# Kernel tuning notes

Hardware: AMD Instinct MI355X
Metric: run time of the kernel (lower is better)

## Reference

```python
import jax, jax.numpy as jnp
import numpy as np

N_NODES = 100000
N_EDGES = 3200000
NEG_SLOPE = 0.2  # PyG GATConv default


def setup_inputs() -> dict:
    key = jax.random.key(0)
    ks = jax.random.split(key, 10)
    x = jax.random.normal(ks[0], (N_NODES, 2), dtype=jnp.float32)
    src = jax.random.randint(ks[1], (N_EDGES,), 0, N_NODES)
    dst = jax.random.randint(ks[2], (N_EDGES,), 0, N_NODES)
    edge_index = jnp.stack([src, dst]).astype(jnp.int64)
    edge_attr = jax.random.normal(ks[3], (N_EDGES, 4), dtype=jnp.float32)
    # layer 1: in=2, heads=4, out_per_head=8
    W1 = jax.random.normal(ks[4], (2, 32), dtype=jnp.float32) * 0.5
    att_src1 = jax.random.normal(ks[5], (4, 8), dtype=jnp.float32) * 0.3
    att_dst1 = jax.random.normal(ks[6], (4, 8), dtype=jnp.float32) * 0.3
    b1 = jnp.zeros((32,), dtype=jnp.float32)
    # layer 2: in=32, heads=1, out_per_head=2
    W2 = jax.random.normal(ks[7], (32, 2), dtype=jnp.float32) * 0.2
    att_src2 = jax.random.normal(ks[8], (1, 2), dtype=jnp.float32) * 0.3
    att_dst2 = jax.random.normal(ks[9], (1, 2), dtype=jnp.float32) * 0.3
    b2 = jnp.zeros((2,), dtype=jnp.float32)
    return {"x": x, "edge_index": edge_index, "edge_attr": edge_attr,
            "W1": W1, "att_src1": att_src1, "att_dst1": att_dst1, "b1": b1,
            "W2": W2, "att_src2": att_src2, "att_dst2": att_dst2, "b2": b2}


def _gat_conv(x, W, att_src, att_dst, bias, src, dst, heads, out_ch, concat, n):
    h = (x @ W).reshape(n, heads, out_ch)            # [N,H,C]
    a_s = (h * att_src).sum(-1)                       # [N,H]
    a_d = (h * att_dst).sum(-1)                       # [N,H]
    e = jax.nn.leaky_relu(a_s[src] + a_d[dst], NEG_SLOPE)  # [E,H]
    m = jax.ops.segment_max(e, dst, num_segments=n)   # stable softmax over dst groups
    ee = jnp.exp(e - m[dst])
    s = jax.ops.segment_sum(ee, dst, num_segments=n)
    alpha = ee / (s[dst] + 1e-16)                     # [E,H]
    out = jax.ops.segment_sum(h[src] * alpha[:, :, None], dst, num_segments=n)  # [N,H,C]
    out = out.reshape(n, heads * out_ch) if concat else out.mean(axis=1)
    return out + bias, alpha


def reference(x, edge_index, edge_attr, W1, att_src1, att_dst1, b1,
              W2, att_src2, att_dst2, b2):
    # edge_attr is accepted but ignored: GATConv was built without edge_dim.
    n = x.shape[0]
    loop = jnp.arange(n, dtype=edge_index.dtype)      # add_self_loops=True (PyG default)
    src = jnp.concatenate([edge_index[0], loop])
    dst = jnp.concatenate([edge_index[1], loop])
    h, alpha1 = _gat_conv(x, W1, att_src1, att_dst1, b1, src, dst, 4, 8, True, n)
    h = jax.nn.elu(h)
    out, alpha2 = _gat_conv(h, W2, att_src2, att_dst2, b2, src, dst, 1, 2, False, n)
    return out, alpha1, alpha2
```

## Files before the change

kernel.cpp:

```cpp
#include <hip/hip_runtime.h>
#include <hip/hip_fp16.h>
#include <math.h>

#define NEG_SLOPE 0.2f
#define BW 512
#define BSH 9
#define CAP 18432
#define NB_MAX 256

typedef float f4v __attribute__((ext_vector_type(4)));
typedef float f2v __attribute__((ext_vector_type(2)));
typedef int   i2v __attribute__((ext_vector_type(2)));

__device__ __forceinline__ float lrelu(float v) {
    return v > 0.0f ? v : NEG_SLOPE * v;
}
__device__ __forceinline__ float pack2h(float a, float b) {
    __half2 h = __floats2half2_rn(a, b);
    return *reinterpret_cast<float*>(&h);
}
__device__ __forceinline__ float2 unpack2h(float f) {
    __half2 h = *reinterpret_cast<__half2*>(&f);
    return __half22float2(h);
}
__device__ __forceinline__ void nt_store4(float4 v, float4* p) {
    f4v x = {v.x, v.y, v.z, v.w};
    __builtin_nontemporal_store(x, (f4v*)p);
}
__device__ __forceinline__ void nt_store2(float2 v, float2* p) {
    f2v x = {v.x, v.y};
    __builtin_nontemporal_store(x, (f2v*)p);
}

__global__ __launch_bounds__(256) void k_l1_node(
    const float* __restrict__ x, const float* __restrict__ W1,
    const float* __restrict__ asw, const float* __restrict__ adw,
    float4* __restrict__ ga, float4* __restrict__ spack,
    float2* __restrict__ dpack2, int* __restrict__ bucketCursor,
    int nb, int n)
{
    int i = blockIdx.x * blockDim.x + threadIdx.x;
    if (i < nb) bucketCursor[i] = 0;
    if (i >= n) return;
    float2 xv = ((const float2*)x)[i];
    float as[4] = {0.f, 0.f, 0.f, 0.f};
    float ad[4] = {0.f, 0.f, 0.f, 0.f};
    #pragma unroll
    for (int j = 0; j < 32; ++j) {
        float h = xv.x * W1[j] + xv.y * W1[32 + j];
        as[j >> 3] += h * asw[j];
        ad[j >> 3] += h * adw[j];
    }
    float p01 = pack2h(as[0], as[1]), p23 = pack2h(as[2], as[3]);
    ga[i] = make_float4(p01, p23, xv.x, xv.y);
    spack[i] = make_float4(p01, p23, 0.f, 0.f);
    dpack2[2 * i] = make_float2(pack2h(ad[0], ad[1]), pack2h(ad[2], ad[3]));
}

__global__ __launch_bounds__(256) void k_binA(
    const int* __restrict__ ei, int* __restrict__ bucketCursor,
    unsigned int* __restrict__ binned, int E, int Et, int nb)
{
    __shared__ int cnt[NB_MAX], lscan[NB_MAX], base[NB_MAX], lcur[NB_MAX];
    __shared__ unsigned int staging[4096];
    __shared__ short sbk[4096];
    int t = threadIdx.x;
    int c0 = blockIdx.x * 4096;
    unsigned int ent[16];
    short bb[16];
    #pragma unroll
    for (int k = 0; k < 16; ++k) {
        int e = c0 + k * 256 + t;
        int s, d;
        if (e < E) {
            s = __builtin_nontemporal_load(&ei[e]);
            d = __builtin_nontemporal_load(&ei[E + e]);
        } else { s = e - E; d = s; }
        bool valid = e < Et;
        bb[k] = valid ? (short)(d >> BSH) : (short)(-1);
        ent[k] = ((unsigned int)s << BSH) | (unsigned int)(d & (BW - 1));
    }
    cnt[t] = 0;
    __syncthreads();
    #pragma unroll
    for (int k = 0; k < 16; ++k)
        if (bb[k] >= 0) atomicAdd(&cnt[bb[k]], 1);
    __syncthreads();
    int c = cnt[t];
    lscan[t] = c;
    __syncthreads();
    for (int off = 1; off < 256; off <<= 1) {
        int v = (t >= off) ? lscan[t - off] : 0;
        __syncthreads();
        lscan[t] += v;
        __syncthreads();
    }
    int tot = lscan[255];
    int ex = lscan[t] - c;
    __syncthreads();
    lscan[t] = ex;
    lcur[t] = ex;
    if (t < nb && c > 0) base[t] = atomicAdd(&bucketCursor[t], c);
    __syncthreads();
    #pragma unroll
    for (int k = 0; k < 16; ++k)
        if (bb[k] >= 0) {
            int p = atomicAdd(&lcur[bb[k]], 1);
            staging[p] = ent[k];
            sbk[p] = bb[k];
        }
    __syncthreads();
    for (int j = t; j < tot; j += 256) {
        int lo = sbk[j];
        __builtin_nontemporal_store(staging[j],
            &binned[(size_t)lo * CAP + base[lo] + (j - lscan[lo])]);
    }
}

__global__ __launch_bounds__(1024) void k_binB(
    const unsigned int* __restrict__ binned, const int* __restrict__ bucketCursor,
    int* __restrict__ sorted, int2* __restrict__ rowrange, int n, int nb)
{
    __shared__ int cnt[BW], cur[BW];
    int t = threadIdx.x;
    int b = blockIdx.x;
    int m = bucketCursor[b];
    size_t base = (size_t)b * CAP;
    int node0 = b << BSH;
    if (t < BW) cnt[t] = 0;
    __syncthreads();
    for (int i = t; i < m; i += 1024)
        atomicAdd(&cnt[binned[base + i] & (BW - 1)], 1);
    __syncthreads();
    int deg = (t < BW) ? cnt[t] : 0;
    for (int off = 1; off < BW; off <<= 1) {
        int v = (t >= off && t < BW) ? cnt[t - off] : 0;
        __syncthreads();
        if (t < BW) cnt[t] += v;
        __syncthreads();
    }
    if (t < BW) {
        int ex = cnt[t] - deg;
        cur[t] = ex;
        int node = node0 + t;
        if (node < n)
            rowrange[node] = make_int2((int)base + ex, (int)base + ex + deg);
    }
    __syncthreads();
    for (int i = t; i < m; i += 1024) {
        unsigned int en = binned[base + i];
        int dl = (int)(en & (BW - 1));
        int p = atomicAdd(&cur[dl], 1);
        sorted[base + p] = (int)(en >> BSH);
    }
}

__global__ __launch_bounds__(256) void k_l1_gather(
    const int2* __restrict__ rowrange, const int* __restrict__ sorted,
    const float4* __restrict__ ga, float2* __restrict__ dpack2,
    const float* __restrict__ W1, const float* __restrict__ b1,
    const float* __restrict__ W2,
    const float* __restrict__ asw2, const float* __restrict__ adw2,
    float4* __restrict__ pk2f, float4* __restrict__ spack,
    __half* __restrict__ dpk2h, int n)
{
    int t = blockIdx.x * blockDim.x + threadIdx.x;
    int d = t >> 1, half = t & 1;
    if (d >= n) return;
    int2 rr = rowrange[d];
    int beg = rr.x, end = rr.y;
    float2 adp = dpack2[2 * d];
    float2 ad01 = unpack2h(adp.x), ad23 = unpack2h(adp.y);
    float see[4] = {0.f, 0.f, 0.f, 0.f};
    float sx0[4] = {0.f, 0.f, 0.f, 0.f};
    float sx1[4] = {0.f, 0.f, 0.f, 0.f};
    int i = beg + half;
    for (; i + 2 < end; i += 4) {
        int s0 = sorted[i], s1 = sorted[i + 2];
        float4 v0 = ga[s0], v1 = ga[s1];
        #pragma unroll
        for (int k = 0; k < 2; ++k) {
            float4 v = k ? v1 : v0;
            float2 a01 = unpack2h(v.x), a23 = unpack2h(v.y);
            float e0 = __expf(lrelu(a01.x + ad01.x));
            float e1 = __expf(lrelu(a01.y + ad01.y));
            float e2 = __expf(lrelu(a23.x + ad23.x));
            float e3 = __expf(lrelu(a23.y + ad23.y));
            see[0] += e0; sx0[0] += e0 * v.z; sx1[0] += e0 * v.w;
            see[1] += e1; sx0[1] += e1 * v.z; sx1[1] += e1 * v.w;
            see[2] += e2; sx0[2] += e2 * v.z; sx1[2] += e2 * v.w;
            see[3] += e3; sx0[3] += e3 * v.z; sx1[3] += e3 * v.w;
        }
    }
    for (; i < end; i += 2) {
        float4 v = ga[sorted[i]];
        float2 a01 = unpack2h(v.x), a23 = unpack2h(v.y);
        float e0 = __expf(lrelu(a01.x + ad01.x));
        float e1 = __expf(lrelu(a01.y + ad01.y));
        float e2 = __expf(lrelu(a23.x + ad23.x));
        float e3 = __expf(lrelu(a23.y + ad23.y));
        see[0] += e0; sx0[0] += e0 * v.z; sx1[0] += e0 * v.w;
        see[1] += e1; sx0[1] += e1 * v.z; sx1[1] += e1 * v.w;
        see[2] += e2; sx0[2] += e2 * v.z; sx1[2] += e2 * v.w;
        see[3] += e3; sx0[3] += e3 * v.z; sx1[3] += e3 * v.w;
    }
    #pragma unroll
    for (int h = 0; h < 4; ++h) {
        see[h] += __shfl_xor(see[h], 1);
        sx0[h] += __shfl_xor(sx0[h], 1);
        sx1[h] += __shfl_xor(sx1[h], 1);
    }
    if (half) return;
    float rs[4];
    #pragma unroll
    for (int h = 0; h < 4; ++h) rs[h] = 1.0f / (see[h] + 1e-16f);
    dpack2[2 * d + 1] = make_float2(pack2h(rs[0], rs[1]), pack2h(rs[2], rs[3]));
    float h20 = 0.f, h21 = 0.f;
    #pragma unroll
    for (int j = 0; j < 32; ++j) {
        int h = j >> 3;
        float num = W1[j] * sx0[h] + W1[32 + j] * sx1[h];
        float o = num * rs[h] + b1[j];
        float he = o > 0.f ? o : expm1f(o);
        h20 += he * W2[2 * j];
        h21 += he * W2[2 * j + 1];
    }
    float as2 = h20 * asw2[0] + h21 * asw2[1];
    float ad2 = h20 * adw2[0] + h21 * adw2[1];
    pk2f[d] = make_float4(as2, h20, h21, ad2);
    ((float*)&spack[d])[2] = as2;
    dpk2h[2 * d] = __float2half(ad2);
}

__global__ __launch_bounds__(256) void k_l2_gather(
    const int2* __restrict__ rowrange, const int* __restrict__ sorted,
    const float4* __restrict__ pk2f, const float* __restrict__ b2,
    __half* __restrict__ dpk2h, float* __restrict__ out, int n)
{
    int t = blockIdx.x * blockDim.x + threadIdx.x;
    int d = t >> 1, half = t & 1;
    if (d >= n) return;
    int2 rr = rowrange[d];
    int beg = rr.x, end = rr.y;
    float ad2 = pk2f[d].w;
    float se = 0.f, a0 = 0.f, a1 = 0.f;
    int i = beg + half;
    for (; i + 2 < end; i += 4) {
        int s0 = sorted[i], s1 = sorted[i + 2];
        float4 p0 = pk2f[s0], p1 = pk2f[s1];
        float e0 = __expf(lrelu(p0.x + ad2));
        float e1 = __expf(lrelu(p1.x + ad2));
        se += e0 + e1;
        a0 += e0 * p0.y + e1 * p1.y;
        a1 += e0 * p0.z + e1 * p1.z;
    }
    for (; i < end; i += 2) {
        float4 p = pk2f[sorted[i]];
        float ee = __expf(lrelu(p.x + ad2));
        se += ee; a0 += ee * p.y; a1 += ee * p.z;
    }
    se += __shfl_xor(se, 1);
    a0 += __shfl_xor(a0, 1);
    a1 += __shfl_xor(a1, 1);
    if (half) return;
    float rs2 = 1.0f / (se + 1e-16f);
    dpk2h[2 * d + 1] = __float2half(rs2);
    ((float2*)out)[d] = make_float2(a0 * rs2 + b2[0], a1 * rs2 + b2[1]);
}

__global__ __launch_bounds__(256) void k_alpha(
    const int* __restrict__ ei, const float4* __restrict__ spack,
    const float4* __restrict__ dpack, const float* __restrict__ dpk2hf,
    float4* __restrict__ alpha1, float2* __restrict__ alpha2_2, int E, int Et)
{
    int p = blockIdx.x * blockDim.x + threadIdx.x;
    int e0 = p * 2;
    if (e0 >= Et) return;
    int s0, d0, s1, d1;
    if (e0 < E) {
        i2v ss = __builtin_nontemporal_load(&((const i2v*)ei)[p]);
        i2v dd = __builtin_nontemporal_load((const i2v*)(ei + E) + (p - E / 2) + E / 2 - E / 2 + (p - 0) - p + p);
        dd = __builtin_nontemporal_load((const i2v*)(ei + E) + p);
        s0 = ss.x; s1 = ss.y; d0 = dd.x; d1 = dd.y;
    } else {
        s0 = e0 - E; d0 = s0; s1 = s0 + 1; d1 = s1;
    }
    float4 sp0 = spack[s0], sp1 = spack[s1];
    float4 dp0 = dpack[d0], dp1 = dpack[d1];
    float  dh0 = dpk2hf[d0], dh1 = dpk2hf[d1];

    float2 a01, a23, b01, b23, r01, r23, ar;
    float4 al;
    a01 = unpack2h(sp0.x); a23 = unpack2h(sp0.y);
    b01 = unpack2h(dp0.x); b23 = unpack2h(dp0.y);
    r01 = unpack2h(dp0.z); r23 = unpack2h(dp0.w);
    al.x = __expf(lrelu(a01.x + b01.x)) * r01.x;
    al.y = __expf(lrelu(a01.y + b01.y)) * r01.y;
    al.z = __expf(lrelu(a23.x + b23.x)) * r23.x;
    al.w = __expf(lrelu(a23.y + b23.y)) * r23.y;
    nt_store4(al, &alpha1[e0]);
    ar = unpack2h(dh0);
    float o20 = __expf(lrelu(sp0.z + ar.x)) * ar.y;
    a01 = unpack2h(sp1.x); a23 = unpack2h(sp1.y);
    b01 = unpack2h(dp1.x); b23 = unpack2h(dp1.y);
    r01 = unpack2h(dp1.z); r23 = unpack2h(dp1.w);
    al.x = __expf(lrelu(a01.x + b01.x)) * r01.x;
    al.y = __expf(lrelu(a01.y + b01.y)) * r01.y;
    al.z = __expf(lrelu(a23.x + b23.x)) * r23.x;
    al.w = __expf(lrelu(a23.y + b23.y)) * r23.y;
    nt_store4(al, &alpha1[e0 + 1]);
    ar = unpack2h(dh1);
    float o21 = __expf(lrelu(sp1.z + ar.x)) * ar.y;
    nt_store2(make_float2(o20, o21), &alpha2_2[p]);
}

extern "C" void kernel_launch(void* const* d_in, const int* in_sizes, int n_in,
                              void* d_out, int out_size, void* d_ws, size_t ws_size,
                              hipStream_t stream)
{
    const float* x   = (const float*)d_in[0];
    const int*   ei  = (const int*)d_in[1];
    const float* W1  = (const float*)d_in[3];
    const float* as1 = (const float*)d_in[4];
    const float* ad1 = (const float*)d_in[5];
    const float* b1  = (const float*)d_in[6];
    const float* W2  = (const float*)d_in[7];
    const float* as2 = (const float*)d_in[8];
    const float* ad2 = (const float*)d_in[9];
    const float* b2  = (const float*)d_in[10];

    const int n  = in_sizes[0] / 2;
    const int E  = in_sizes[1] / 2;
    const int Et = E + n;
    const int nb = (n + BW - 1) >> BSH;

    char* w = (char*)d_ws;
    float4* ga    = (float4*)w;  w += (size_t)n * sizeof(float4);
    float4* spack = (float4*)w;  w += (size_t)n * sizeof(float4);
    float4* dpack = (float4*)w;  w += (size_t)n * sizeof(float4);
    float4* pk2f  = (float4*)w;  w += (size_t)n * sizeof(float4);
    float*  dpk2hf= (float*)w;   w += (size_t)n * sizeof(float);
    int2*   rowrange = (int2*)w; w += (size_t)n * sizeof(int2);
    int*    sorted   = (int*)w;  w += (size_t)nb * CAP * sizeof(int);
    int*    bucketCursor = (int*)w; w += (size_t)nb * sizeof(int);

    float*  out    = (float*)d_out;
    float4* alpha1 = (float4*)(out + (size_t)n * 2);
    float2* alpha2_2 = (float2*)(alpha1 + (size_t)Et);
    unsigned int* binned = (unsigned int*)alpha1;

    dim3 blk(256);
    int gn   = (n + 255) / 256;
    int gn2  = (2 * n + 255) / 256;
    int gA   = (Et + 4095) / 4096;
    int gP   = (Et / 2 + 255) / 256;

    k_l1_node  <<<gn,  blk, 0, stream>>>(x, W1, as1, ad1, ga, spack,
                                         (float2*)dpack, bucketCursor, nb, n);
    k_binA     <<<gA,  blk, 0, stream>>>(ei, bucketCursor, binned, E, Et, nb);
    k_binB     <<<nb, dim3(1024), 0, stream>>>(binned, bucketCursor, sorted, rowrange, n, nb);
    k_l1_gather<<<gn2, blk, 0, stream>>>(rowrange, sorted, ga, (float2*)dpack,
                                         W1, b1, W2, as2, ad2, pk2f, spack,
                                         (__half*)dpk2hf, n);
    k_l2_gather<<<gn2, blk, 0, stream>>>(rowrange, sorted, pk2f, b2,
                                         (__half*)dpk2hf, out, n);
    k_alpha    <<<gP,  blk, 0, stream>>>(ei, spack, dpack, dpk2hf,
                                         alpha1, alpha2_2, E, Et);
}
```

Before: 291.6 us.

## Merge per-destination alpha data into one 32-byte record and stage alpha1 stores through LDS

Combines the destination-side layer-1 record (attention logits plus reciprocal sums) and the layer-2 dst logit/reciprocal into one 32-byte per-node record. The layer-2 pair is now stored in fp32 rather than half. Each random gather in k_alpha then touches one contiguous region instead of two separate arrays. k_alpha also writes its alpha1 results to shared memory and then stores them so consecutive lanes write consecutive float4s. The cost is a doubled dpk footprint, a block barrier and some LDS traffic.

```diff
diff --git a/kernel.cpp b/kernel.cpp
--- a/kernel.cpp
+++ b/kernel.cpp
@@ -36,7 +36,7 @@
     const float* __restrict__ x, const float* __restrict__ W1,
     const float* __restrict__ asw, const float* __restrict__ adw,
     float4* __restrict__ ga, float4* __restrict__ spack,
-    float2* __restrict__ dpack2, int* __restrict__ bucketCursor,
+    float4* __restrict__ dpk, int* __restrict__ bucketCursor,
     int nb, int n)
 {
     int i = blockIdx.x * blockDim.x + threadIdx.x;
@@ -54,7 +54,7 @@
     float p01 = pack2h(as[0], as[1]), p23 = pack2h(as[2], as[3]);
     ga[i] = make_float4(p01, p23, xv.x, xv.y);
     spack[i] = make_float4(p01, p23, 0.f, 0.f);
-    dpack2[2 * i] = make_float2(pack2h(ad[0], ad[1]), pack2h(ad[2], ad[3]));
+    dpk[2 * i] = make_float4(pack2h(ad[0], ad[1]), pack2h(ad[2], ad[3]), 0.f, 0.f);
 }
 
 __global__ __launch_bounds__(256) void k_binA(
@@ -157,19 +157,18 @@
 
 __global__ __launch_bounds__(256) void k_l1_gather(
     const int2* __restrict__ rowrange, const int* __restrict__ sorted,
-    const float4* __restrict__ ga, float2* __restrict__ dpack2,
+    const float4* __restrict__ ga, float4* __restrict__ dpk,
     const float* __restrict__ W1, const float* __restrict__ b1,
     const float* __restrict__ W2,
     const float* __restrict__ asw2, const float* __restrict__ adw2,
-    float4* __restrict__ pk2f, float4* __restrict__ spack,
-    __half* __restrict__ dpk2h, int n)
+    float4* __restrict__ pk2f, float4* __restrict__ spack, int n)
 {
     int t = blockIdx.x * blockDim.x + threadIdx.x;
     int d = t >> 1, half = t & 1;
     if (d >= n) return;
     int2 rr = rowrange[d];
     int beg = rr.x, end = rr.y;
-    float2 adp = dpack2[2 * d];
+    float2 adp = *(const float2*)&dpk[2 * d];
     float2 ad01 = unpack2h(adp.x), ad23 = unpack2h(adp.y);
     float see[4] = {0.f, 0.f, 0.f, 0.f};
     float sx0[4] = {0.f, 0.f, 0.f, 0.f};
@@ -214,7 +213,7 @@
     float rs[4];
     #pragma unroll
     for (int h = 0; h < 4; ++h) rs[h] = 1.0f / (see[h] + 1e-16f);
-    dpack2[2 * d + 1] = make_float2(pack2h(rs[0], rs[1]), pack2h(rs[2], rs[3]));
+    ((float2*)&dpk[2 * d])[1] = make_float2(pack2h(rs[0], rs[1]), pack2h(rs[2], rs[3]));
     float h20 = 0.f, h21 = 0.f;
     #pragma unroll
     for (int j = 0; j < 32; ++j) {
@@ -229,13 +228,13 @@
     float ad2 = h20 * adw2[0] + h21 * adw2[1];
     pk2f[d] = make_float4(as2, h20, h21, ad2);
     ((float*)&spack[d])[2] = as2;
-    dpk2h[2 * d] = __float2half(ad2);
+    ((float*)&dpk[2 * d + 1])[0] = ad2;
 }
 
 __global__ __launch_bounds__(256) void k_l2_gather(
     const int2* __restrict__ rowrange, const int* __restrict__ sorted,
     const float4* __restrict__ pk2f, const float* __restrict__ b2,
-    __half* __restrict__ dpk2h, float* __restrict__ out, int n)
+    float4* __restrict__ dpk, float* __restrict__ out, int n)
 {
     int t = blockIdx.x * blockDim.x + threadIdx.x;
     int d = t >> 1, half = t & 1;
@@ -264,54 +263,62 @@
     a1 += __shfl_xor(a1, 1);
     if (half) return;
     float rs2 = 1.0f / (se + 1e-16f);
-    dpk2h[2 * d + 1] = __float2half(rs2);
+    ((float*)&dpk[2 * d + 1])[1] = rs2;
     ((float2*)out)[d] = make_float2(a0 * rs2 + b2[0], a1 * rs2 + b2[1]);
 }
 
 __global__ __launch_bounds__(256) void k_alpha(
     const int* __restrict__ ei, const float4* __restrict__ spack,
-    const float4* __restrict__ dpack, const float* __restrict__ dpk2hf,
+    const float4* __restrict__ dpk,
     float4* __restrict__ alpha1, float2* __restrict__ alpha2_2, int E, int Et)
 {
-    int p = blockIdx.x * blockDim.x + threadIdx.x;
-    int e0 = p * 2;
-    if (e0 >= Et) return;
-    int s0, d0, s1, d1;
-    if (e0 < E) {
-        i2v ss = __builtin_nontemporal_load(&((const i2v*)ei)[p]);
-        i2v dd = __builtin_nontemporal_load((const i2v*)(ei + E) + (p - E / 2) + E / 2 - E / 2 + (p - 0) - p + p);
-        dd = __builtin_nontemporal_load((const i2v*)(ei + E) + p);
-        s0 = ss.x; s1 = ss.y; d0 = dd.x; d1 = dd.y;
-    } else {
-        s0 = e0 - E; d0 = s0; s1 = s0 + 1; d1 = s1;
-    }
-    float4 sp0 = spack[s0], sp1 = spack[s1];
-    float4 dp0 = dpack[d0], dp1 = dpack[d1];
-    float  dh0 = dpk2hf[d0], dh1 = dpk2hf[d1];
-
-    float2 a01, a23, b01, b23, r01, r23, ar;
-    float4 al;
-    a01 = unpack2h(sp0.x); a23 = unpack2h(sp0.y);
-    b01 = unpack2h(dp0.x); b23 = unpack2h(dp0.y);
-    r01 = unpack2h(dp0.z); r23 = unpack2h(dp0.w);
-    al.x = __expf(lrelu(a01.x + b01.x)) * r01.x;
-    al.y = __expf(lrelu(a01.y + b01.y)) * r01.y;
-    al.z = __expf(lrelu(a23.x + b23.x)) * r23.x;
-    al.w = __expf(lrelu(a23.y + b23.y)) * r23.y;
-    nt_store4(al, &alpha1[e0]);
-    ar = unpack2h(dh0);
-    float o20 = __expf(lrelu(sp0.z + ar.x)) * ar.y;
-    a01 = unpack2h(sp1.x); a23 = unpack2h(sp1.y);
-    b01 = unpack2h(dp1.x); b23 = unpack2h(dp1.y);
-    r01 = unpack2h(dp1.z); r23 = unpack2h(dp1.w);
-    al.x = __expf(lrelu(a01.x + b01.x)) * r01.x;
-    al.y = __expf(lrelu(a01.y + b01.y)) * r01.y;
-    al.z = __expf(lrelu(a23.x + b23.x)) * r23.x;
-    al.w = __expf(lrelu(a23.y + b23.y)) * r23.y;
-    nt_store4(al, &alpha1[e0 + 1]);
-    ar = unpack2h(dh1);
-    float o21 = __expf(lrelu(sp1.z + ar.x)) * ar.y;
-    nt_store2(make_float2(o20, o21), &alpha2_2[p]);
+    __shared__ float4 lds[512];
+    int t = threadIdx.x;
+    int base = blockIdx.x * 512;
+    int e0 = base + 2 * t;
+    if (e0 < Et) {
+        int s0, d0, s1, d1;
+        if (e0 < E) {
+            i2v ss = __builtin_nontemporal_load((const i2v*)(ei + e0));
+            i2v dd = __builtin_nontemporal_load((const i2v*)(ei + E + e0));
+            s0 = ss.x; s1 = ss.y; d0 = dd.x; d1 = dd.y;
+        } else {
+            s0 = e0 - E; d0 = s0; s1 = s0 + 1; d1 = s1;
+        }
+        float4 sp0 = spack[s0], sp1 = spack[s1];
+        float4 dA0 = dpk[2 * d0], dA1 = dpk[2 * d1];
+        float2 dB0 = *(const float2*)&dpk[2 * d0 + 1];
+        float2 dB1 = *(const float2*)&dpk[2 * d1 + 1];
+
+        float2 a01, a23, b01, b23, r01, r23;
+        float4 al;
+        a01 = unpack2h(sp0.x); a23 = unpack2h(sp0.y);
+        b01 = unpack2h(dA0.x); b23 = unpack2h(dA0.y);
+        r01 = unpack2h(dA0.z); r23 = unpack2h(dA0.w);
+        al.x = __expf(lrelu(a01.x + b01.x)) * r01.x;
+        al.y = __expf(lrelu(a01.y + b01.y)) * r01.y;
+        al.z = __expf(lrelu(a23.x + b23.x)) * r23.x;
+        al.w = __expf(lrelu(a23.y + b23.y)) * r23.y;
+        lds[t] = al;
+        float o20 = __expf(lrelu(sp0.z + dB0.x)) * dB0.y;
+        a01 = unpack2h(sp1.x); a23 = unpack2h(sp1.y);
+        b01 = unpack2h(dA1.x); b23 = unpack2h(dA1.y);
+        r01 = unpack2h(dA1.z); r23 = unpack2h(dA1.w);
+        al.x = __expf(lrelu(a01.x + b01.x)) * r01.x;
+        al.y = __expf(lrelu(a01.y + b01.y)) * r01.y;
+        al.z = __expf(lrelu(a23.x + b23.x)) * r23.x;
+        al.w = __expf(lrelu(a23.y + b23.y)) * r23.y;
+        lds[256 + t] = al;
+        float o21 = __expf(lrelu(sp1.z + dB1.x)) * dB1.y;
+        nt_store2(make_float2(o20, o21), &alpha2_2[(base >> 1) + t]);
+    }
+    __syncthreads();
+    int v0 = t;
+    if (base + v0 < Et)
+        nt_store4(lds[(v0 & 1) * 256 + (v0 >> 1)], &alpha1[base + v0]);
+    int v1 = t + 256;
+    if (base + v1 < Et)
+        nt_store4(lds[(v1 & 1) * 256 + 128 + (v1 >> 1) - 128], &alpha1[base + v1]);
 }
 
 extern "C" void kernel_launch(void* const* d_in, const int* in_sizes, int n_in,
@@ -337,9 +344,8 @@
     char* w = (char*)d_ws;
     float4* ga    = (float4*)w;  w += (size_t)n * sizeof(float4);
     float4* spack = (float4*)w;  w += (size_t)n * sizeof(float4);
-    float4* dpack = (float4*)w;  w += (size_t)n * sizeof(float4);
+    float4* dpk   = (float4*)w;  w += (size_t)n * 2 * sizeof(float4);
     float4* pk2f  = (float4*)w;  w += (size_t)n * sizeof(float4);
-    float*  dpk2hf= (float*)w;   w += (size_t)n * sizeof(float);
     int2*   rowrange = (int2*)w; w += (size_t)n * sizeof(int2);
     int*    sorted   = (int*)w;  w += (size_t)nb * CAP * sizeof(int);
     int*    bucketCursor = (int*)w; w += (size_t)nb * sizeof(int);
@@ -353,17 +359,16 @@
     int gn   = (n + 255) / 256;
     int gn2  = (2 * n + 255) / 256;
     int gA   = (Et + 4095) / 4096;
-    int gP   = (Et / 2 + 255) / 256;
+    int gAl  = (Et + 511) / 512;
 
     k_l1_node  <<<gn,  blk, 0, stream>>>(x, W1, as1, ad1, ga, spack,
-                                         (float2*)dpack, bucketCursor, nb, n);
+                                         dpk, bucketCursor, nb, n);
     k_binA     <<<gA,  blk, 0, stream>>>(ei, bucketCursor, binned, E, Et, nb);
     k_binB     <<<nb, dim3(1024), 0, stream>>>(binned, bucketCursor, sorted, rowrange, n, nb);
-    k_l1_gather<<<gn2, blk, 0, stream>>>(rowrange, sorted, ga, (float2*)dpack,
-                                         W1, b1, W2, as2, ad2, pk2f, spack,
-                                         (__half*)dpk2hf, n);
+    k_l1_gather<<<gn2, blk, 0, stream>>>(rowrange, sorted, ga, dpk,
+                                         W1, b1, W2, as2, ad2, pk2f, spack, n);
     k_l2_gather<<<gn2, blk, 0, stream>>>(rowrange, sorted, pk2f, b2,
-                                         (__half*)dpk2hf, out, n);
-    k_alpha    <<<gP,  blk, 0, stream>>>(ei, spack, dpack, dpk2hf,
+                                         dpk, out, n);
+    k_alpha    <<<gAl, blk, 0, stream>>>(ei, spack, dpk,
                                          alpha1, alpha2_2, E, Et);
 }
```

After: 289.7 us. No clear change (-0.7%).

## Use 8 lanes per node in gathers and stage alpha1 stores through LDS

Applied to the files above, without the earlier changes.

Both gather kernels now give each destination node 8 lanes instead of 2 and reduce the partial sums with three xor-shuffle steps. This spreads the ~33 edges per node across more threads for more memory-level parallelism. The alpha kernel now writes alpha1 into shared memory first and then issues contiguous, coalesced float4 nontemporal stores, instead of each thread storing to two strided positions. The costs are 4x more threads in the gathers, extra shuffle work, and a block barrier plus 8KB of LDS in the alpha kernel.

```diff
diff --git a/kernel.cpp b/kernel.cpp
--- a/kernel.cpp
+++ b/kernel.cpp
@@ -165,7 +165,7 @@
     __half* __restrict__ dpk2h, int n)
 {
     int t = blockIdx.x * blockDim.x + threadIdx.x;
-    int d = t >> 1, half = t & 1;
+    int d = t >> 3, q = t & 7;
     if (d >= n) return;
     int2 rr = rowrange[d];
     int beg = rr.x, end = rr.y;
@@ -174,9 +174,9 @@
     float see[4] = {0.f, 0.f, 0.f, 0.f};
     float sx0[4] = {0.f, 0.f, 0.f, 0.f};
     float sx1[4] = {0.f, 0.f, 0.f, 0.f};
-    int i = beg + half;
-    for (; i + 2 < end; i += 4) {
-        int s0 = sorted[i], s1 = sorted[i + 2];
+    int i = beg + q;
+    for (; i + 8 < end; i += 16) {
+        int s0 = sorted[i], s1 = sorted[i + 8];
         float4 v0 = ga[s0], v1 = ga[s1];
         #pragma unroll
         for (int k = 0; k < 2; ++k) {
@@ -192,7 +192,7 @@
             see[3] += e3; sx0[3] += e3 * v.z; sx1[3] += e3 * v.w;
         }
     }
-    for (; i < end; i += 2) {
+    for (; i < end; i += 8) {
         float4 v = ga[sorted[i]];
         float2 a01 = unpack2h(v.x), a23 = unpack2h(v.y);
         float e0 = __expf(lrelu(a01.x + ad01.x));
@@ -209,8 +209,14 @@
         see[h] += __shfl_xor(see[h], 1);
         sx0[h] += __shfl_xor(sx0[h], 1);
         sx1[h] += __shfl_xor(sx1[h], 1);
-    }
-    if (half) return;
+        see[h] += __shfl_xor(see[h], 2);
+        sx0[h] += __shfl_xor(sx0[h], 2);
+        sx1[h] += __shfl_xor(sx1[h], 2);
+        see[h] += __shfl_xor(see[h], 4);
+        sx0[h] += __shfl_xor(sx0[h], 4);
+        sx1[h] += __shfl_xor(sx1[h], 4);
+    }
+    if (q) return;
     float rs[4];
     #pragma unroll
     for (int h = 0; h < 4; ++h) rs[h] = 1.0f / (see[h] + 1e-16f);
@@ -238,15 +244,15 @@
     __half* __restrict__ dpk2h, float* __restrict__ out, int n)
 {
     int t = blockIdx.x * blockDim.x + threadIdx.x;
-    int d = t >> 1, half = t & 1;
+    int d = t >> 3, q = t & 7;
     if (d >= n) return;
     int2 rr = rowrange[d];
     int beg = rr.x, end = rr.y;
     float ad2 = pk2f[d].w;
     float se = 0.f, a0 = 0.f, a1 = 0.f;
-    int i = beg + half;
-    for (; i + 2 < end; i += 4) {
-        int s0 = sorted[i], s1 = sorted[i + 2];
+    int i = beg + q;
+    for (; i + 8 < end; i += 16) {
+        int s0 = sorted[i], s1 = sorted[i + 8];
         float4 p0 = pk2f[s0], p1 = pk2f[s1];
         float e0 = __expf(lrelu(p0.x + ad2));
         float e1 = __expf(lrelu(p1.x + ad2));
@@ -254,15 +260,15 @@
         a0 += e0 * p0.y + e1 * p1.y;
         a1 += e0 * p0.z + e1 * p1.z;
     }
-    for (; i < end; i += 2) {
+    for (; i < end; i += 8) {
         float4 p = pk2f[sorted[i]];
         float ee = __expf(lrelu(p.x + ad2));
         se += ee; a0 += ee * p.y; a1 += ee * p.z;
     }
-    se += __shfl_xor(se, 1);
-    a0 += __shfl_xor(a0, 1);
-    a1 += __shfl_xor(a1, 1);
-    if (half) return;
+    se += __shfl_xor(se, 1); a0 += __shfl_xor(a0, 1); a1 += __shfl_xor(a1, 1);
+    se += __shfl_xor(se, 2); a0 += __shfl_xor(a0, 2); a1 += __shfl_xor(a1, 2);
+    se += __shfl_xor(se, 4); a0 += __shfl_xor(a0, 4); a1 += __shfl_xor(a1, 4);
+    if (q) return;
     float rs2 = 1.0f / (se + 1e-16f);
     dpk2h[2 * d + 1] = __float2half(rs2);
     ((float2*)out)[d] = make_float2(a0 * rs2 + b2[0], a1 * rs2 + b2[1]);
@@ -273,45 +279,54 @@
     const float4* __restrict__ dpack, const float* __restrict__ dpk2hf,
     float4* __restrict__ alpha1, float2* __restrict__ alpha2_2, int E, int Et)
 {
-    int p = blockIdx.x * blockDim.x + threadIdx.x;
-    int e0 = p * 2;
-    if (e0 >= Et) return;
-    int s0, d0, s1, d1;
-    if (e0 < E) {
-        i2v ss = __builtin_nontemporal_load(&((const i2v*)ei)[p]);
-        i2v dd = __builtin_nontemporal_load((const i2v*)(ei + E) + (p - E / 2) + E / 2 - E / 2 + (p - 0) - p + p);
-        dd = __builtin_nontemporal_load((const i2v*)(ei + E) + p);
-        s0 = ss.x; s1 = ss.y; d0 = dd.x; d1 = dd.y;
-    } else {
-        s0 = e0 - E; d0 = s0; s1 = s0 + 1; d1 = s1;
-    }
-    float4 sp0 = spack[s0], sp1 = spack[s1];
-    float4 dp0 = dpack[d0], dp1 = dpack[d1];
-    float  dh0 = dpk2hf[d0], dh1 = dpk2hf[d1];
-
-    float2 a01, a23, b01, b23, r01, r23, ar;
-    float4 al;
-    a01 = unpack2h(sp0.x); a23 = unpack2h(sp0.y);
-    b01 = unpack2h(dp0.x); b23 = unpack2h(dp0.y);
-    r01 = unpack2h(dp0.z); r23 = unpack2h(dp0.w);
-    al.x = __expf(lrelu(a01.x + b01.x)) * r01.x;
-    al.y = __expf(lrelu(a01.y + b01.y)) * r01.y;
-    al.z = __expf(lrelu(a23.x + b23.x)) * r23.x;
-    al.w = __expf(lrelu(a23.y + b23.y)) * r23.y;
-    nt_store4(al, &alpha1[e0]);
-    ar = unpack2h(dh0);
-    float o20 = __expf(lrelu(sp0.z + ar.x)) * ar.y;
-    a01 = unpack2h(sp1.x); a23 = unpack2h(sp1.y);
-    b01 = unpack2h(dp1.x); b23 = unpack2h(dp1.y);
-    r01 = unpack2h(dp1.z); r23 = unpack2h(dp1.w);
-    al.x = __expf(lrelu(a01.x + b01.x)) * r01.x;
-    al.y = __expf(lrelu(a01.y + b01.y)) * r01.y;
-    al.z = __expf(lrelu(a23.x + b23.x)) * r23.x;
-    al.w = __expf(lrelu(a23.y + b23.y)) * r23.y;
-    nt_store4(al, &alpha1[e0 + 1]);
-    ar = unpack2h(dh1);
-    float o21 = __expf(lrelu(sp1.z + ar.x)) * ar.y;
-    nt_store2(make_float2(o20, o21), &alpha2_2[p]);
+    __shared__ float4 lds[512];
+    int t = threadIdx.x;
+    int base = blockIdx.x * 512;
+    int e0 = base + 2 * t;
+    if (e0 < Et) {
+        int s0, d0, s1, d1;
+        if (e0 < E) {
+            i2v ss = __builtin_nontemporal_load((const i2v*)(ei + e0));
+            i2v dd = __builtin_nontemporal_load((const i2v*)(ei + E + e0));
+            s0 = ss.x; s1 = ss.y; d0 = dd.x; d1 = dd.y;
+        } else {
+            s0 = e0 - E; d0 = s0; s1 = s0 + 1; d1 = s1;
+        }
+        float4 sp0 = spack[s0], sp1 = spack[s1];
+        float4 dp0 = dpack[d0], dp1 = dpack[d1];
+        float  dh0 = dpk2hf[d0], dh1 = dpk2hf[d1];
+
+        float2 a01, a23, b01, b23, r01, r23, ar;
+        float4 al;
+        a01 = unpack2h(sp0.x); a23 = unpack2h(sp0.y);
+        b01 = unpack2h(dp0.x); b23 = unpack2h(dp0.y);
+        r01 = unpack2h(dp0.z); r23 = unpack2h(dp0.w);
+        al.x = __expf(lrelu(a01.x + b01.x)) * r01.x;
+        al.y = __expf(lrelu(a01.y + b01.y)) * r01.y;
+        al.z = __expf(lrelu(a23.x + b23.x)) * r23.x;
+        al.w = __expf(lrelu(a23.y + b23.y)) * r23.y;
+        lds[t] = al;
+        ar = unpack2h(dh0);
+        float o20 = __expf(lrelu(sp0.z + ar.x)) * ar.y;
+        a01 = unpack2h(sp1.x); a23 = unpack2h(sp1.y);
+        b01 = unpack2h(dp1.x); b23 = unpack2h(dp1.y);
+        r01 = unpack2h(dp1.z); r23 = unpack2h(dp1.w);
+        al.x = __expf(lrelu(a01.x + b01.x)) * r01.x;
+        al.y = __expf(lrelu(a01.y + b01.y)) * r01.y;
+        al.z = __expf(lrelu(a23.x + b23.x)) * r23.x;
+        al.w = __expf(lrelu(a23.y + b23.y)) * r23.y;
+        lds[256 + t] = al;
+        ar = unpack2h(dh1);
+        float o21 = __expf(lrelu(sp1.z + ar.x)) * ar.y;
+        nt_store2(make_float2(o20, o21), &alpha2_2[(base >> 1) + t]);
+    }
+    __syncthreads();
+    int v0 = t;
+    if (base + v0 < Et)
+        nt_store4(lds[(v0 & 1) * 256 + (v0 >> 1)], &alpha1[base + v0]);
+    int v1 = t + 256;
+    if (base + v1 < Et)
+        nt_store4(lds[(v1 & 1) * 256 + (v1 >> 1)], &alpha1[base + v1]);
 }
 
 extern "C" void kernel_launch(void* const* d_in, const int* in_sizes, int n_in,
@@ -351,19 +366,19 @@
 
     dim3 blk(256);
     int gn   = (n + 255) / 256;
-    int gn2  = (2 * n + 255) / 256;
+    int gn8  = (8 * n + 255) / 256;
     int gA   = (Et + 4095) / 4096;
-    int gP   = (Et / 2 + 255) / 256;
+    int gAl  = (Et + 511) / 512;
 
     k_l1_node  <<<gn,  blk, 0, stream>>>(x, W1, as1, ad1, ga, spack,
                                          (float2*)dpack, bucketCursor, nb, n);
     k_binA     <<<gA,  blk, 0, stream>>>(ei, bucketCursor, binned, E, Et, nb);
     k_binB     <<<nb, dim3(1024), 0, stream>>>(binned, bucketCursor, sorted, rowrange, n, nb);
-    k_l1_gather<<<gn2, blk, 0, stream>>>(rowrange, sorted, ga, (float2*)dpack,
+    k_l1_gather<<<gn8, blk, 0, stream>>>(rowrange, sorted, ga, (float2*)dpack,
                                          W1, b1, W2, as2, ad2, pk2f, spack,
                                          (__half*)dpk2hf, n);
-    k_l2_gather<<<gn2, blk, 0, stream>>>(rowrange, sorted, pk2f, b2,
+    k_l2_gather<<<gn8, blk, 0, stream>>>(rowrange, sorted, pk2f, b2,
                                          (__half*)dpk2hf, out, n);
-    k_alpha    <<<gP,  blk, 0, stream>>>(ei, spack, dpack, dpk2hf,
+    k_alpha    <<<gAl, blk, 0, stream>>>(ei, spack, dpack, dpk2hf,
                                          alpha1, alpha2_2, E, Et);
 }
```

Result: faster. 284.3 us (-2.5%).
